# Optimization experiments

Hardware: AMD Instinct MI355X
Metric: run time of the kernel (lower is better)

Reference implementation:

```python
import jax, jax.numpy as jnp
import numpy as np

DIM = 768
NUM_PROMPTS = 10
LATENT = 20
B = 16
N = 4096
EPS = 1e-5


def quick_gelu(x):
    return x * jax.nn.sigmoid(1.702 * x)


def layer_norm(x, g, b):
    mu = jnp.mean(x, axis=-1, keepdims=True)
    var = jnp.var(x, axis=-1, keepdims=True)
    return (x - mu) * jax.lax.rsqrt(var + EPS) * g + b


def setup_inputs() -> dict:
    key = jax.random.key(0)
    ks = jax.random.split(key, 12)
    s_in = 1.0 / np.sqrt(DIM)
    s_lat = 1.0 / np.sqrt(LATENT)
    s64 = 1.0 / np.sqrt(64)
    return {
        "x": jax.random.normal(ks[0], (B, NUM_PROMPTS + 1 + N, DIM), jnp.float32),
        "local_tokens": jax.random.normal(ks[1], (B, N, DIM), jnp.float32),
        # proj_down: Linear(dim, latent)
        "Wd": jax.random.uniform(ks[2], (DIM, LATENT), jnp.float32, -s_in, s_in),
        "bd": jnp.zeros((LATENT,), jnp.float32),
        # proj_up: Linear(latent, dim)
        "Wu": jax.random.uniform(ks[3], (LATENT, DIM), jnp.float32, -s_lat, s_lat),
        "bu": jnp.zeros((DIM,), jnp.float32),
        # global / local query projections: Linear(latent, latent)
        "Wgq": jax.random.uniform(ks[4], (LATENT, LATENT), jnp.float32, -s_lat, s_lat),
        "bgq": jnp.zeros((LATENT,), jnp.float32),
        "Wlq": jax.random.uniform(ks[5], (LATENT, LATENT), jnp.float32, -s_lat, s_lat),
        "blq": jnp.zeros((LATENT,), jnp.float32),
        # cls_analyzer: LN(latent) -> Linear(latent,64) -> GELU -> Linear(64,num_prompts) -> Sigmoid
        "ln_c_g": jnp.ones((LATENT,), jnp.float32),
        "ln_c_b": jnp.zeros((LATENT,), jnp.float32),
        "Wc1": jax.random.uniform(ks[6], (LATENT, 64), jnp.float32, -s_lat, s_lat),
        "bc1": jnp.zeros((64,), jnp.float32),
        "Wc2": jax.random.uniform(ks[7], (64, NUM_PROMPTS), jnp.float32, -s64, s64),
        "bc2": jnp.zeros((NUM_PROMPTS,), jnp.float32),
        # gl_balancer: LN(latent) -> Linear(latent,1) -> Sigmoid
        "ln_g_g": jnp.ones((LATENT,), jnp.float32),
        "ln_g_b": jnp.zeros((LATENT,), jnp.float32),
        "Wg": jax.random.uniform(ks[8], (LATENT, 1), jnp.float32, -s_lat, s_lat),
        "bg": jnp.zeros((1,), jnp.float32),
    }


def _attend(q, tokens, scale):
    # q: [B,P,d], tokens: [B,n,d]
    w = jax.nn.softmax(jnp.einsum('bpd,bnd->bpn', q, tokens) * scale, axis=-1)
    return jnp.einsum('bpn,bnd->bpd', w, tokens)


def reference(x, local_tokens, Wd, bd, Wu, bu, Wgq, bgq, Wlq, blq,
              ln_c_g, ln_c_b, Wc1, bc1, Wc2, bc2, ln_g_g, ln_g_b, Wg, bg):
    scale = LATENT ** (-0.5)
    x_latent = quick_gelu(x @ Wd + bd)            # [B, P+1+N, d]
    local_latent = quick_gelu(local_tokens @ Wd + bd)  # [B, N, d]

    prompts_latent = x_latent[:, :NUM_PROMPTS]              # [B,P,d]
    cls_latent = x_latent[:, NUM_PROMPTS:NUM_PROMPTS + 1]   # [B,1,d]
    global_img_latent = x_latent[:, NUM_PROMPTS + 1:]       # [B,N,d]

    cls_ln = layer_norm(cls_latent, ln_c_g, ln_c_b)
    prompt_importance = jax.nn.sigmoid(
        jax.nn.gelu(cls_ln @ Wc1 + bc1, approximate=False) @ Wc2 + bc2)  # [B,1,P]
    global_weight = jax.nn.sigmoid(layer_norm(cls_latent, ln_g_g, ln_g_b) @ Wg + bg)  # [B,1,1]

    global_context = _attend(prompts_latent @ Wgq + bgq, global_img_latent, scale)
    local_context = _attend(prompts_latent @ Wlq + blq, local_latent, scale)

    fused = global_weight * global_context + (1.0 - global_weight) * local_context
    enhanced = fused * jnp.swapaxes(prompt_importance, 1, 2)  # [B,P,d]

    combined = jnp.concatenate([enhanced, cls_latent, global_img_latent], axis=1)
    return combined @ Wu + bu
```

## Files before the change

### kernel.cpp

```cpp
#include <hip/hip_runtime.h>
#include <math.h>

#define DIM   768
#define LAT   20
#define NP    10
#define NB    16
#define SEQ   4096
#define SEQX  (NP + 1 + SEQ)
#define NXROWS (NB * SEQX)
#define NLROWS (NB * SEQ)
#define NROWS  (NXROWS + NLROWS)
#define EPSF  1e-5f

typedef __attribute__((ext_vector_type(8))) short  v8s;
typedef __attribute__((ext_vector_type(4))) float  v4f;
typedef __attribute__((ext_vector_type(4))) unsigned short u16x4;
typedef __attribute__((ext_vector_type(8))) unsigned short u16x8;

__device__ __forceinline__ float sigmoidf_(float z) { return 1.f / (1.f + __expf(-z)); }

__device__ __forceinline__ unsigned short bf16u(float v) {
    unsigned u = __builtin_bit_cast(unsigned, v);
    unsigned r = u + 0x7fffu + ((u >> 16) & 1u);
    return (unsigned short)(r >> 16);
}

#define WF_US   24576
#define XBUF_US 8192
__global__ __launch_bounds__(256, 2) void k_down(const float* __restrict__ x,
                                                 const float* __restrict__ loc,
                                                 const float* __restrict__ Wd,
                                                 const float* __restrict__ bd,
                                                 float* __restrict__ lat)
{
    __shared__ __align__(16) unsigned short lds[WF_US + 2 * XBUF_US];
    const int tid = threadIdx.x;
    const int rowbase = blockIdx.x * 64;

    for (int slot = tid; slot < 3072; slot += 256) {
        int fs = slot >> 7;
        int rem = slot & 127;
        int nt = rem >> 6, l = rem & 63;
        int n = nt * 16 + (l & 15);
        int q = l >> 4;
        u16x8 w;
#pragma unroll
        for (int e = 0; e < 8; e++) {
            int k = fs * 32 + q * 8 + e;
            float v = (n < LAT) ? Wd[k * LAT + n] : 0.f;
            w[e] = bf16u(v);
        }
        *(u16x8*)&lds[((fs * 2 + nt) * 64 + l) * 8] = w;
    }

    auto stage = [&](int c, int b) {
        const int base = WF_US + b * XBUF_US;
#pragma unroll
        for (int i = 0; i < 8; i++) {
            int g = tid + 256 * i;
            int row_l = g >> 5, fq = g & 31;
            int kc = fq << 2;
            int row = rowbase + row_l;
            float4 f = make_float4(0.f, 0.f, 0.f, 0.f);
            if (row < NROWS) {
                const float* src = (row < NXROWS) ? x + (size_t)row * DIM
                                                  : loc + (size_t)(row - NXROWS) * DIM;
                f = *(const float4*)(src + c * 128 + kc);
            }
            int s = kc >> 5, q = (kc >> 3) & 3, e = kc & 7;
            int t = row_l >> 4, m = row_l & 15;
            int lane = q * 16 + m;
            u16x4 u = { bf16u(f.x), bf16u(f.y), bf16u(f.z), bf16u(f.w) };
            *(u16x4*)&lds[base + ((s * 4 + t) * 64 + lane) * 8 + e] = u;
        }
    };

    stage(0, 0);
    __syncthreads();

    const int t = tid >> 6, l = tid & 63;
    v4f acc0 = {0.f, 0.f, 0.f, 0.f}, acc1 = {0.f, 0.f, 0.f, 0.f};

    for (int c = 0; c < 6; c++) {
        if (c < 5) stage(c + 1, (c + 1) & 1);
        const int base = WF_US + (c & 1) * XBUF_US;
#pragma unroll
        for (int s = 0; s < 4; s++) {
            v8s a  = *(const v8s*)&lds[base + ((s * 4 + t) * 64 + l) * 8];
            int fs = c * 4 + s;
            v8s b0 = *(const v8s*)&lds[((fs * 2 + 0) * 64 + l) * 8];
            v8s b1 = *(const v8s*)&lds[((fs * 2 + 1) * 64 + l) * 8];
            acc0 = __builtin_amdgcn_mfma_f32_16x16x32_bf16(a, b0, acc0, 0, 0, 0);
            acc1 = __builtin_amdgcn_mfma_f32_16x16x32_bf16(a, b1, acc1, 0, 0, 0);
        }
        __syncthreads();
    }

    int col = l & 15, half = l >> 4;
#pragma unroll
    for (int nt = 0; nt < 2; nt++) {
        int j = nt * 16 + col;
        if (j >= LAT) continue;
        float bdj = bd[j];
        v4f A = nt ? acc1 : acc0;
#pragma unroll
        for (int r = 0; r < 4; r++) {
            int rowg = rowbase + t * 16 + half * 4 + r;
            if (rowg < NROWS) {
                float z = A[r] + bdj;
                lat[(size_t)rowg * LAT + j] = z * sigmoidf_(1.702f * z);
            }
        }
    }
}

__global__ __launch_bounds__(192, 3) void k_up(const float* __restrict__ lat,
                                               const float* __restrict__ Wu,
                                               const float* __restrict__ bu,
                                               float* __restrict__ out)
{
    int t = threadIdx.x;
    float4 wu[LAT];
#pragma unroll
    for (int k = 0; k < LAT; k++) wu[k] = ((const float4*)Wu)[k * 192 + t];
    float4 bv = ((const float4*)bu)[t];

    __shared__ float latile[64 * LAT];
    int rowbase = blockIdx.x * 64;
    {
        const float4* src = (const float4*)(lat + (size_t)rowbase * LAT);
        for (int idx = t; idx < 320; idx += 192) ((float4*)latile)[idx] = src[idx];
    }
    __syncthreads();

    int idx0 = rowbase % SEQX;
    for (int i = 0; i < 64; i++) {
        int row = rowbase + i;
        if (row >= NXROWS) break;
        int idx = idx0 + i;
        if (idx >= SEQX) idx -= SEQX;
        if (idx < NP) continue;
        const float* lp = latile + i * LAT;
        float4 acc = bv;
#pragma unroll
        for (int k = 0; k < LAT; k++) {
            float v = lp[k];
            acc.x += v * wu[k].x; acc.y += v * wu[k].y;
            acc.z += v * wu[k].z; acc.w += v * wu[k].w;
        }
        ((float4*)out)[(size_t)row * 192 + t] = acc;
    }
}

__global__ __launch_bounds__(64) void k_small(const float* __restrict__ lat_x,
    const float* __restrict__ Wgq, const float* __restrict__ bgq,
    const float* __restrict__ Wlq, const float* __restrict__ blq,
    const float* __restrict__ lncg, const float* __restrict__ lncb,
    const float* __restrict__ Wc1, const float* __restrict__ bc1,
    const float* __restrict__ Wc2, const float* __restrict__ bc2,
    const float* __restrict__ lngg, const float* __restrict__ lngb,
    const float* __restrict__ Wg, const float* __restrict__ bg,
    float* __restrict__ qg, float* __restrict__ ql,
    float* __restrict__ imp, float* __restrict__ gw)
{
    int b = blockIdx.x, t = threadIdx.x;
    __shared__ float cls[LAT], clsln[LAT], h1[64];
    __shared__ float mu_s, rs_s;

    const float* cp = lat_x + (size_t)(b * SEQX + NP) * LAT;
    if (t < LAT) cls[t] = cp[t];
    __syncthreads();

    if (t == 0) {
        float m = 0.f;
        for (int k = 0; k < LAT; k++) m += cls[k];
        m /= LAT;
        float v = 0.f;
        for (int k = 0; k < LAT; k++) { float d = cls[k] - m; v += d * d; }
        v /= LAT;
        float rs = rsqrtf(v + EPSF);
        mu_s = m; rs_s = rs;
        float s = bg[0];
        for (int k = 0; k < LAT; k++)
            s += ((cls[k] - m) * rs * lngg[k] + lngb[k]) * Wg[k];
        gw[b] = sigmoidf_(s);
    }
    __syncthreads();
    if (t < LAT) clsln[t] = (cls[t] - mu_s) * rs_s * lncg[t] + lncb[t];
    __syncthreads();

    {
        float s = bc1[t];
        for (int k = 0; k < LAT; k++) s += clsln[k] * Wc1[k * 64 + t];
        h1[t] = 0.5f * s * (1.f + erff(s * 0.70710678118f));
    }
    __syncthreads();
    if (t < NP) {
        float s = bc2[t];
        for (int i = 0; i < 64; i++) s += h1[i] * Wc2[i * NP + t];
        imp[b * NP + t] = sigmoidf_(s);
    }
    for (int idx = t; idx < NP * LAT; idx += 64) {
        int p = idx / LAT, j = idx % LAT;
        const float* pl = lat_x + (size_t)(b * SEQX + p) * LAT;
        float sg = bgq[j], sl = blq[j];
        for (int k = 0; k < LAT; k++) {
            float v = pl[k];
            sg += v * Wgq[k * LAT + j];
            sl += v * Wlq[k * LAT + j];
        }
        qg[(b * NP + p) * LAT + j] = sg;
        ql[(b * NP + p) * LAT + j] = sl;
    }
}

__global__ __launch_bounds__(256) void k_attn(const float* __restrict__ lat_x,
                                              const float* __restrict__ lat_l,
                                              const float* __restrict__ qg,
                                              const float* __restrict__ ql,
                                              float* __restrict__ ctxg,
                                              float* __restrict__ ctxl)
{
    int b = blockIdx.x, p = blockIdx.y, ty = blockIdx.z;
    const float* tok = (ty == 0) ? lat_x + (size_t)(b * SEQX + NP + 1) * LAT
                                 : lat_l + (size_t)b * SEQ * LAT;
    const float* q = ((ty == 0) ? qg : ql) + (size_t)(b * NP + p) * LAT;
    float* ctx = ((ty == 0) ? ctxg : ctxl) + (size_t)(b * NP + p) * LAT;

    int t = threadIdx.x;
    __shared__ float qs[LAT];
    __shared__ float red[128];
    __shared__ float Ms;
    __shared__ float tot[21];
    if (t < LAT) qs[t] = q[t];
    __syncthreads();

    const float scale = 0.22360679775f;
    float lg[16];
    float lmax = -1e30f;
    for (int i = 0; i < 16; i++) {
        const float* tk = tok + (size_t)(t + 256 * i) * LAT;
        float s = 0.f;
#pragma unroll
        for (int k = 0; k < LAT; k++) s += qs[k] * tk[k];
        s *= scale;
        lg[i] = s;
        lmax = fmaxf(lmax, s);
    }
    int wave = t >> 6, lane = t & 63;
    for (int off = 32; off; off >>= 1) lmax = fmaxf(lmax, __shfl_down(lmax, off, 64));
    if (lane == 0) red[wave] = lmax;
    __syncthreads();
    if (t == 0) Ms = fmaxf(fmaxf(red[0], red[1]), fmaxf(red[2], red[3]));
    __syncthreads();
    float M = Ms;

    float vals[21];
#pragma unroll
    for (int j = 0; j < 21; j++) vals[j] = 0.f;
    for (int i = 0; i < 16; i++) {
        float w = __expf(lg[i] - M);
        vals[20] += w;
        const float* tk = tok + (size_t)(t + 256 * i) * LAT;
#pragma unroll
        for (int k = 0; k < LAT; k++) vals[k] += w * tk[k];
    }
#pragma unroll
    for (int j = 0; j < 21; j++) {
        float v = vals[j];
        for (int off = 32; off; off >>= 1) v += __shfl_down(v, off, 64);
        vals[j] = v;
    }
    __syncthreads();
    if (lane == 0)
        for (int j = 0; j < 21; j++) red[wave * 21 + j] = vals[j];
    __syncthreads();
    if (t < 21) tot[t] = red[t] + red[21 + t] + red[42 + t] + red[63 + t];
    __syncthreads();
    if (t < LAT) ctx[t] = tot[t] / tot[20];
}

__global__ __launch_bounds__(192) void k_prompt_out(const float* __restrict__ ctxg,
                                                    const float* __restrict__ ctxl,
                                                    const float* __restrict__ imp,
                                                    const float* __restrict__ gw,
                                                    const float* __restrict__ Wu,
                                                    const float* __restrict__ bu,
                                                    float* __restrict__ out)
{
    int b = blockIdx.x, p = blockIdx.y, t = threadIdx.x;
    __shared__ float enh[LAT];
    if (t < LAT) {
        float g = gw[b];
        size_t o = (size_t)(b * NP + p) * LAT + t;
        float e = g * ctxg[o] + (1.f - g) * ctxl[o];
        enh[t] = e * imp[b * NP + p];
    }
    __syncthreads();
    float4 acc = ((const float4*)bu)[t];
#pragma unroll
    for (int k = 0; k < LAT; k++) {
        float4 w = ((const float4*)Wu)[k * 192 + t];
        float e = enh[k];
        acc.x += e * w.x; acc.y += e * w.y; acc.z += e * w.z; acc.w += e * w.w;
    }
    ((float4*)out)[(size_t)(b * SEQX + p) * 192 + t] = acc;
}

extern "C" void kernel_launch(void* const* d_in, const int* in_sizes, int n_in,
                              void* d_out, int out_size, void* d_ws, size_t ws_size,
                              hipStream_t stream)
{
    const float* x    = (const float*)d_in[0];
    const float* loc  = (const float*)d_in[1];
    const float* Wd   = (const float*)d_in[2];
    const float* bd   = (const float*)d_in[3];
    const float* Wu   = (const float*)d_in[4];
    const float* bu   = (const float*)d_in[5];
    const float* Wgq  = (const float*)d_in[6];
    const float* bgq  = (const float*)d_in[7];
    const float* Wlq  = (const float*)d_in[8];
    const float* blq  = (const float*)d_in[9];
    const float* lncg = (const float*)d_in[10];
    const float* lncb = (const float*)d_in[11];
    const float* Wc1  = (const float*)d_in[12];
    const float* bc1  = (const float*)d_in[13];
    const float* Wc2  = (const float*)d_in[14];
    const float* bc2  = (const float*)d_in[15];
    const float* lngg = (const float*)d_in[16];
    const float* lngb = (const float*)d_in[17];
    const float* Wg   = (const float*)d_in[18];
    const float* bg   = (const float*)d_in[19];
    float* out = (float*)d_out;

    float* ws   = (float*)d_ws;
    float* lat_x = ws;
    float* lat_l = lat_x + (size_t)NXROWS * LAT;
    float* qg    = lat_l + (size_t)NLROWS * LAT;
    float* ql    = qg + NB * NP * LAT;
    float* ctxg  = ql + NB * NP * LAT;
    float* ctxl  = ctxg + NB * NP * LAT;
    float* impw  = ctxl + NB * NP * LAT;
    float* gww   = impw + NB * NP;

    k_down<<<(NROWS + 63) / 64, 256, 0, stream>>>(x, loc, Wd, bd, lat_x);
    k_up<<<(NXROWS + 63) / 64, 192, 0, stream>>>(lat_x, Wu, bu, out);
    k_small<<<NB, 64, 0, stream>>>(lat_x, Wgq, bgq, Wlq, blq, lncg, lncb,
                                   Wc1, bc1, Wc2, bc2, lngg, lngb, Wg, bg,
                                   qg, ql, impw, gww);
    k_attn<<<dim3(NB, NP, 2), 256, 0, stream>>>(lat_x, lat_l, qg, ql, ctxg, ctxl);
    k_prompt_out<<<dim3(NB, NP), 192, 0, stream>>>(ctxg, ctxl, impw, gww, Wu, bu, out);
}
```

Before: 639.6 us.

## Stream down-projection inputs via async global-to-LDS ring and precomputed weight fragments

Moves the bf16 conversion and fragment packing of Wd into a separate small kernel, so each k_down block only copies ready-made fragments into LDS. It also replaces the block-wide double-buffered staging with a per-wave 4-slot ring filled by global_load_lds, using explicit vmcnt waits to keep several loads in flight without block barriers. The activation-to-bf16 conversion now happens in registers just before each MFMA. The cost is an extra kernel launch, larger LDS use per block, and hand-tuned waitcnt sequencing that depends on the exact load counts.

```diff
diff --git a/kernel.cpp b/kernel.cpp
--- a/kernel.cpp
+++ b/kernel.cpp
@@ -25,76 +25,102 @@
     return (unsigned short)(r >> 16);
 }
 
-#define WF_US   24576
-#define XBUF_US 8192
+__device__ __forceinline__ void gload_lds16(const void* g, void* s) {
+    __builtin_amdgcn_global_load_lds(
+        (const __attribute__((address_space(1))) unsigned int*)g,
+        (__attribute__((address_space(3))) unsigned int*)s, 16, 0, 0);
+}
+
+__global__ __launch_bounds__(256) void k_wfrag(const float* __restrict__ Wd,
+                                               unsigned short* __restrict__ wf)
+{
+    int slot = blockIdx.x * 256 + threadIdx.x;
+    int fs = slot >> 7, rem = slot & 127;
+    int nt = rem >> 6, l = rem & 63;
+    int n = nt * 16 + (l & 15);
+    int q = l >> 4;
+    u16x8 w;
+#pragma unroll
+    for (int e = 0; e < 8; e++) {
+        int k = fs * 32 + q * 8 + e;
+        float v = (n < LAT) ? Wd[k * LAT + n] : 0.f;
+        w[e] = bf16u(v);
+    }
+    *(u16x8*)&wf[slot * 8] = w;
+}
+
+#define WF_B    49152
+#define SLOT_B  2048
+#define RING_B  (4 * SLOT_B)
+
 __global__ __launch_bounds__(256, 2) void k_down(const float* __restrict__ x,
                                                  const float* __restrict__ loc,
-                                                 const float* __restrict__ Wd,
+                                                 const unsigned short* __restrict__ wf,
                                                  const float* __restrict__ bd,
                                                  float* __restrict__ lat)
 {
-    __shared__ __align__(16) unsigned short lds[WF_US + 2 * XBUF_US];
-    const int tid = threadIdx.x;
-    const int rowbase = blockIdx.x * 64;
-
-    for (int slot = tid; slot < 3072; slot += 256) {
-        int fs = slot >> 7;
-        int rem = slot & 127;
-        int nt = rem >> 6, l = rem & 63;
-        int n = nt * 16 + (l & 15);
-        int q = l >> 4;
-        u16x8 w;
-#pragma unroll
-        for (int e = 0; e < 8; e++) {
-            int k = fs * 32 + q * 8 + e;
-            float v = (n < LAT) ? Wd[k * LAT + n] : 0.f;
-            w[e] = bf16u(v);
+    __shared__ __align__(16) unsigned short lds[(WF_B + 4 * RING_B) / 2];
+    const int tid = threadIdx.x, l = tid & 63, w = tid >> 6;
+
+    {
+        const char* g = (const char*)wf;
+        char* s = (char*)lds;
+#pragma unroll
+        for (int i = 0; i < 12; ++i) {
+            int off = i * 4096 + w * 1024;
+            gload_lds16(g + off + l * 16, s + off);
         }
-        *(u16x8*)&lds[((fs * 2 + nt) * 64 + l) * 8] = w;
-    }
-
-    auto stage = [&](int c, int b) {
-        const int base = WF_US + b * XBUF_US;
-#pragma unroll
-        for (int i = 0; i < 8; i++) {
-            int g = tid + 256 * i;
-            int row_l = g >> 5, fq = g & 31;
-            int kc = fq << 2;
-            int row = rowbase + row_l;
-            float4 f = make_float4(0.f, 0.f, 0.f, 0.f);
-            if (row < NROWS) {
-                const float* src = (row < NXROWS) ? x + (size_t)row * DIM
-                                                  : loc + (size_t)(row - NXROWS) * DIM;
-                f = *(const float4*)(src + c * 128 + kc);
-            }
-            int s = kc >> 5, q = (kc >> 3) & 3, e = kc & 7;
-            int t = row_l >> 4, m = row_l & 15;
-            int lane = q * 16 + m;
-            u16x4 u = { bf16u(f.x), bf16u(f.y), bf16u(f.z), bf16u(f.w) };
-            *(u16x4*)&lds[base + ((s * 4 + t) * 64 + lane) * 8 + e] = u;
-        }
-    };
-
-    stage(0, 0);
-    __syncthreads();
-
-    const int t = tid >> 6, l = tid & 63;
+    }
+    asm volatile("s_waitcnt vmcnt(0)" ::: "memory");
+    __syncthreads();
+
+    const int r0 = blockIdx.x * 64 + w * 16;
+    if (r0 >= NROWS) return;
+    const float* srcb = (r0 < NXROWS) ? x + (size_t)r0 * DIM
+                                      : loc + (size_t)(r0 - NXROWS) * DIM;
+    const float* gp = srcb + (size_t)(l & 15) * DIM + (l >> 4) * 8;
+    char* ring = (char*)lds + WF_B + w * RING_B;
+
+#pragma unroll
+    for (int p = 0; p < 4; ++p) {
+        gload_lds16(gp + p * 32,     ring + p * SLOT_B);
+        gload_lds16(gp + p * 32 + 4, ring + p * SLOT_B + 1024);
+    }
+
     v4f acc0 = {0.f, 0.f, 0.f, 0.f}, acc1 = {0.f, 0.f, 0.f, 0.f};
 
-    for (int c = 0; c < 6; c++) {
-        if (c < 5) stage(c + 1, (c + 1) & 1);
-        const int base = WF_US + (c & 1) * XBUF_US;
-#pragma unroll
-        for (int s = 0; s < 4; s++) {
-            v8s a  = *(const v8s*)&lds[base + ((s * 4 + t) * 64 + l) * 8];
-            int fs = c * 4 + s;
-            v8s b0 = *(const v8s*)&lds[((fs * 2 + 0) * 64 + l) * 8];
-            v8s b1 = *(const v8s*)&lds[((fs * 2 + 1) * 64 + l) * 8];
-            acc0 = __builtin_amdgcn_mfma_f32_16x16x32_bf16(a, b0, acc0, 0, 0, 0);
-            acc1 = __builtin_amdgcn_mfma_f32_16x16x32_bf16(a, b1, acc1, 0, 0, 0);
-        }
-        __syncthreads();
-    }
+#define CVT8(A, F0, F1)                                                   \
+    A[0] = (short)bf16u(F0.x); A[1] = (short)bf16u(F0.y);                 \
+    A[2] = (short)bf16u(F0.z); A[3] = (short)bf16u(F0.w);                 \
+    A[4] = (short)bf16u(F1.x); A[5] = (short)bf16u(F1.y);                 \
+    A[6] = (short)bf16u(F1.z); A[7] = (short)bf16u(F1.w);
+
+#define KSTEP(T, VMSTR) do {                                              \
+    asm volatile("s_waitcnt " VMSTR ::: "memory");                        \
+    float4 f0 = *(const float4*)(ring + ((T) & 3) * SLOT_B + l * 16);     \
+    float4 f1 = *(const float4*)(ring + ((T) & 3) * SLOT_B + 1024 + l * 16); \
+    v8s a; CVT8(a, f0, f1);                                               \
+    v8s b0 = *(const v8s*)&lds[(((T) * 2 + 0) * 64 + l) * 8];             \
+    v8s b1 = *(const v8s*)&lds[(((T) * 2 + 1) * 64 + l) * 8];             \
+    acc0 = __builtin_amdgcn_mfma_f32_16x16x32_bf16(a, b0, acc0, 0, 0, 0); \
+    acc1 = __builtin_amdgcn_mfma_f32_16x16x32_bf16(a, b1, acc1, 0, 0, 0); \
+    if ((T) + 4 < 24) {                                                   \
+        asm volatile("s_waitcnt lgkmcnt(0)" ::: "memory");                \
+        gload_lds16(gp + ((T) + 4) * 32,     ring + ((T) & 3) * SLOT_B);  \
+        gload_lds16(gp + ((T) + 4) * 32 + 4, ring + ((T) & 3) * SLOT_B + 1024); \
+    }                                                                     \
+} while (0)
+
+    KSTEP(0,  "vmcnt(6)");  KSTEP(1,  "vmcnt(6)");  KSTEP(2,  "vmcnt(6)");
+    KSTEP(3,  "vmcnt(6)");  KSTEP(4,  "vmcnt(6)");  KSTEP(5,  "vmcnt(6)");
+    KSTEP(6,  "vmcnt(6)");  KSTEP(7,  "vmcnt(6)");  KSTEP(8,  "vmcnt(6)");
+    KSTEP(9,  "vmcnt(6)");  KSTEP(10, "vmcnt(6)");  KSTEP(11, "vmcnt(6)");
+    KSTEP(12, "vmcnt(6)");  KSTEP(13, "vmcnt(6)");  KSTEP(14, "vmcnt(6)");
+    KSTEP(15, "vmcnt(6)");  KSTEP(16, "vmcnt(6)");  KSTEP(17, "vmcnt(6)");
+    KSTEP(18, "vmcnt(6)");  KSTEP(19, "vmcnt(6)");  KSTEP(20, "vmcnt(6)");
+    KSTEP(21, "vmcnt(4)");  KSTEP(22, "vmcnt(2)");  KSTEP(23, "vmcnt(0)");
+#undef KSTEP
+#undef CVT8
 
     int col = l & 15, half = l >> 4;
 #pragma unroll
@@ -105,11 +131,9 @@
         v4f A = nt ? acc1 : acc0;
 #pragma unroll
         for (int r = 0; r < 4; r++) {
-            int rowg = rowbase + t * 16 + half * 4 + r;
-            if (rowg < NROWS) {
-                float z = A[r] + bdj;
-                lat[(size_t)rowg * LAT + j] = z * sigmoidf_(1.702f * z);
-            }
+            int rowg = r0 + half * 4 + r;
+            float z = A[r] + bdj;
+            lat[(size_t)rowg * LAT + j] = z * sigmoidf_(1.702f * z);
         }
     }
 }
@@ -342,8 +366,10 @@
     float* ctxl  = ctxg + NB * NP * LAT;
     float* impw  = ctxl + NB * NP * LAT;
     float* gww   = impw + NB * NP;
-
-    k_down<<<(NROWS + 63) / 64, 256, 0, stream>>>(x, loc, Wd, bd, lat_x);
+    unsigned short* wfrag = (unsigned short*)(gww + NB);
+
+    k_wfrag<<<12, 256, 0, stream>>>(Wd, wfrag);
+    k_down<<<(NROWS + 63) / 64, 256, 0, stream>>>(x, loc, wfrag, bd, lat_x);
     k_up<<<(NXROWS + 63) / 64, 192, 0, stream>>>(lat_x, Wu, bu, out);
     k_small<<<NB, 64, 0, stream>>>(lat_x, Wgq, bgq, Wlq, blq, lncg, lncb,
                                    Wc1, bc1, Wc2, bc2, lngg, lngb, Wg, bg,
```

Result: faster. 566.3 us (-11.5%).
